# Kernel tuning notes

Hardware: AMD Instinct MI355X
Metric: run time of the kernel (lower is better)

The kernel has to match this reference:

```python
import jax, jax.numpy as jnp
import numpy as np

N = 4_194_304          # total events
C = 16                 # n classes
SIGNAL_CLS = 0         # signal_cls_idx
EPS = 1.0              # self.eps
B_BG = 2_097_152       # background rows (rows [0, B_BG) are background, rest signal)
N_SIG_SEG = 4          # len(idx['signal'])
N_BG_SEG = 8           # len(idx['background'])


def setup_inputs() -> dict:
    key = jax.random.key(0)
    k1, k2, k3, k4 = jax.random.split(key, 4)
    pred = jax.random.normal(k1, (N, C), dtype=jnp.float32)
    n_sig = N - B_BG
    # truth layout required by split_signal_and_background: background rows first
    # (class != SIGNAL_CLS), then signal rows (class == SIGNAL_CLS), one-hot.
    bg_cls = jax.random.randint(k2, (B_BG,), 1, C).astype(jnp.int32)
    sig_cls = jnp.full((n_sig,), SIGNAL_CLS, dtype=jnp.int32)
    truth = jax.nn.one_hot(jnp.concatenate([bg_cls, sig_cls]), C, dtype=jnp.float32)
    weight_signal = jax.random.uniform(k3, (N_SIG_SEG,), dtype=jnp.float32)
    weight_background = jax.random.uniform(k4, (N_BG_SEG,), dtype=jnp.float32)
    # equal-length contiguous segments (cumsum-slice structure of idx lists)
    signal_seg_ids = jnp.repeat(jnp.arange(N_SIG_SEG, dtype=jnp.int32), n_sig // N_SIG_SEG)
    background_seg_ids = jnp.repeat(jnp.arange(N_BG_SEG, dtype=jnp.int32), B_BG // N_BG_SEG)
    return {
        "pred": pred,
        "truth": truth,
        "weight_signal": weight_signal,
        "weight_background": weight_background,
        "signal_seg_ids": signal_seg_ids,
        "background_seg_ids": background_seg_ids,
        "signal_start": B_BG,
    }


def reference(pred, truth, weight_signal, weight_background,
              signal_seg_ids, background_seg_ids, signal_start):
    pred_cls = jnp.argmax(pred, axis=1)    # [N]
    truth_cls = jnpp_argmax = jnp.argmax(truth, axis=1)

    # ---- signal_score: per-segment efficiency * weight ----
    sig_pred_cls = pred_cls[signal_start:]
    sig_truth_cls = truth_cls[signal_start:]
    mism = (sig_pred_cls != sig_truth_cls).astype(jnp.float32)
    fn = jax.ops.segment_sum(mism, signal_seg_ids, num_segments=N_SIG_SEG)
    cnt = jax.ops.segment_sum(jnp.ones_like(mism), signal_seg_ids, num_segments=N_SIG_SEG)
    signal_fraction_score = jnp.sum((cnt - fn) / cnt * weight_signal)

    # ---- background_scores: sqrt(rate_into_signal * w + eps) per segment ----
    bg_pred_cls = pred_cls[:signal_start]
    hit = (bg_pred_cls == SIGNAL_CLS).astype(jnp.float32)
    fns = jax.ops.segment_sum(hit, background_seg_ids, num_segments=N_BG_SEG)
    cnt_b = jax.ops.segment_sum(jnp.ones_like(hit), background_seg_ids, num_segments=N_BG_SEG)
    background_fraction_score = jnp.sum(jnp.sqrt(fns / cnt_b * weight_background + EPS))

    max_score = jnp.sum(weight_signal) / jnp.sqrt(jnp.float32(EPS))
    coefficient = (max_score - signal_fraction_score) / background_fraction_score

    # base loss: mean softmax cross-entropy with soft (one-hot) targets
    loss = jnp.mean(-jnp.sum(truth * jax.nn.log_softmax(pred, axis=1), axis=1))
    return loss * coefficient
```

## Files before the change

### kernel.cpp

```cpp
#include <hip/hip_runtime.h>


__global__ void init_ws(double* loss_sum, unsigned int* ctr) {
    if (threadIdx.x == 0) *loss_sum = 0.0;
    if (threadIdx.x < 24) ctr[threadIdx.x] = 0u;
}

__global__ __launch_bounds__(256) void zscore_main(
    const float4* __restrict__ pred,
    const float4* __restrict__ truth,
    const int*    __restrict__ sig_ids,
    const int*    __restrict__ bg_ids,
    int N, int signal_start,
    double* __restrict__ loss_sum,
    unsigned int* __restrict__ ctr)
{
    __shared__ unsigned int s_flag[12];
    __shared__ unsigned int s_cnt[12];
    __shared__ float s_wave_loss[4];

    const int tid = threadIdx.x;
    if (tid < 12) { s_flag[tid] = 0u; s_cnt[tid] = 0u; }
    __syncthreads();

    const int T = gridDim.x * blockDim.x;
    float local_loss = 0.0f;

    for (int row = blockIdx.x * blockDim.x + tid; row < N; row += T) {
        const float4* pr = pred  + (size_t)row * 4;
        const float4* tr = truth + (size_t)row * 4;
        float4 p0 = pr[0], p1 = pr[1], p2 = pr[2], p3 = pr[3];
        float4 t0 = tr[0], t1 = tr[1], t2 = tr[2], t3 = tr[3];

        float v[16] = {p0.x,p0.y,p0.z,p0.w, p1.x,p1.y,p1.z,p1.w,
                       p2.x,p2.y,p2.z,p2.w, p3.x,p3.y,p3.z,p3.w};
        float t[16] = {t0.x,t0.y,t0.z,t0.w, t1.x,t1.y,t1.z,t1.w,
                       t2.x,t2.y,t2.z,t2.w, t3.x,t3.y,t3.z,t3.w};

        float pm = v[0]; int am = 0;
        #pragma unroll
        for (int i = 1; i < 16; ++i) { if (v[i] > pm) { pm = v[i]; am = i; } }

        float tmx = t[0]; int tm = 0;
        #pragma unroll
        for (int i = 1; i < 16; ++i) { if (t[i] > tmx) { tmx = t[i]; tm = i; } }

        float s = 0.0f;
        #pragma unroll
        for (int i = 0; i < 16; ++i) s += __expf(v[i] - pm);
        float lse = pm + __logf(s);

        float pv = v[0];
        #pragma unroll
        for (int i = 1; i < 16; ++i) pv = (i == tm) ? v[i] : pv;

        local_loss += lse - pv;

        bool isSig = row >= signal_start;
        int p; bool flag;
        if (isSig) { p = sig_ids[row - signal_start]; flag = (am != tm); }
        else       { p = 4 + bg_ids[row];             flag = (am == 0);  }

        int p0l = __builtin_amdgcn_readfirstlane(p);
        bool uni = __all(p == p0l);
        if (uni) {
            unsigned long long fb = __ballot(flag);
            unsigned long long ab = __ballot(true);
            if ((tid & 63) == 0) {
                atomicAdd(&s_cnt[p0l],  (unsigned int)__popcll(ab));
                atomicAdd(&s_flag[p0l], (unsigned int)__popcll(fb));
            }
        } else {
            atomicAdd(&s_cnt[p], 1u);
            if (flag) atomicAdd(&s_flag[p], 1u);
        }
    }

    #pragma unroll
    for (int off = 32; off > 0; off >>= 1)
        local_loss += __shfl_down(local_loss, off);
    if ((tid & 63) == 0) s_wave_loss[tid >> 6] = local_loss;
    __syncthreads();

    if (tid == 0) {
        float bl = s_wave_loss[0] + s_wave_loss[1] + s_wave_loss[2] + s_wave_loss[3];
        atomicAdd(loss_sum, (double)bl);
    }
    if (tid < 12) {
        int fIdx = (tid < 4) ? tid       : 8  + (tid - 4);
        int cIdx = (tid < 4) ? 4 + tid   : 16 + (tid - 4);
        if (s_flag[tid]) atomicAdd(&ctr[fIdx], s_flag[tid]);
        if (s_cnt[tid])  atomicAdd(&ctr[cIdx], s_cnt[tid]);
    }
}

__global__ void finalize(const float* __restrict__ w_sig,
                         const float* __restrict__ w_bg,
                         const double* __restrict__ loss_sum,
                         const unsigned int* __restrict__ ctr,
                         float* __restrict__ out, int N)
{
    if (threadIdx.x != 0 || blockIdx.x != 0) return;
    double sig = 0.0, wsum = 0.0;
    for (int s = 0; s < 4; ++s) {
        double cnt = (double)ctr[4 + s];
        double fn  = (double)ctr[s];
        sig  += (cnt - fn) / cnt * (double)w_sig[s];
        wsum += (double)w_sig[s];
    }
    double bg = 0.0;
    for (int s = 0; s < 8; ++s) {
        double fns = (double)ctr[8 + s];
        double cb  = (double)ctr[16 + s];
        bg += sqrt(fns / cb * (double)w_bg[s] + 1.0);
    }
    double coeff = (wsum - sig) / bg;
    double loss  = (*loss_sum) / (double)N;
    out[0] = (float)(loss * coeff);
}

extern "C" void kernel_launch(void* const* d_in, const int* in_sizes, int n_in,
                              void* d_out, int out_size, void* d_ws, size_t ws_size,
                              hipStream_t stream) {
    const float* pred   = (const float*)d_in[0];
    const float* truth  = (const float*)d_in[1];
    const float* w_sig  = (const float*)d_in[2];
    const float* w_bg   = (const float*)d_in[3];
    const int*   sigid  = (const int*)d_in[4];
    const int*   bgid   = (const int*)d_in[5];

    const int N = in_sizes[0] / 16;
    const int signal_start = in_sizes[5];

    double*       loss_sum = (double*)d_ws;
    unsigned int* ctr      = (unsigned int*)((char*)d_ws + 8);

    init_ws<<<1, 64, 0, stream>>>(loss_sum, ctr);

    const int blocks = 1024;
    zscore_main<<<blocks, 256, 0, stream>>>(
        (const float4*)pred, (const float4*)truth, sigid, bgid,
        N, signal_start, loss_sum, ctr);

    finalize<<<1, 64, 0, stream>>>(w_sig, w_bg, loss_sum, ctr, (float*)d_out, N);
}
```

Before: 537.1 us.

## Split each row across four lanes with coalesced float4 loads and per-block partials

Each row of 16 floats is now handled by four adjacent lanes, each loading one float4, so global loads are fully coalesced instead of each thread reading 64 contiguous bytes. Max, exp-sum and the target logit are combined across the lane quad with xor shuffles, and the next iteration's loads are prefetched one step ahead. Global atomics and the init kernel are replaced by per-block partial arrays reduced in a wider finalize kernel, dropping one launch. The cost is extra shuffles per row and redundant segment-id loads across the four lanes of a quad. The argmax check now uses float equality, so ties behave differently from the first-index rule.

```diff
diff --git a/kernel.cpp b/kernel.cpp
--- a/kernel.cpp
+++ b/kernel.cpp
@@ -1,122 +1,155 @@
 #include <hip/hip_runtime.h>
 
 
-__global__ void init_ws(double* loss_sum, unsigned int* ctr) {
-    if (threadIdx.x == 0) *loss_sum = 0.0;
-    if (threadIdx.x < 24) ctr[threadIdx.x] = 0u;
-}
+#define NBLK 2048
 
-__global__ __launch_bounds__(256) void zscore_main(
-    const float4* __restrict__ pred,
-    const float4* __restrict__ truth,
+__global__ __launch_bounds__(256, 8) void zscore_main(
+    const float4* __restrict__ pred4,
+    const float4* __restrict__ truth4,
     const int*    __restrict__ sig_ids,
     const int*    __restrict__ bg_ids,
     int N, int signal_start,
-    double* __restrict__ loss_sum,
-    unsigned int* __restrict__ ctr)
+    float* __restrict__ lossP,
+    unsigned int* __restrict__ ctrP)
 {
     __shared__ unsigned int s_flag[12];
     __shared__ unsigned int s_cnt[12];
     __shared__ float s_wave_loss[4];
 
-    const int tid = threadIdx.x;
+    const int tid  = threadIdx.x;
+    const int lane = tid & 63;
+    const int j    = tid & 3;
     if (tid < 12) { s_flag[tid] = 0u; s_cnt[tid] = 0u; }
     __syncthreads();
 
     const int T = gridDim.x * blockDim.x;
+    const int totalF = N * 4;
     float local_loss = 0.0f;
 
-    for (int row = blockIdx.x * blockDim.x + tid; row < N; row += T) {
-        const float4* pr = pred  + (size_t)row * 4;
-        const float4* tr = truth + (size_t)row * 4;
-        float4 p0 = pr[0], p1 = pr[1], p2 = pr[2], p3 = pr[3];
-        float4 t0 = tr[0], t1 = tr[1], t2 = tr[2], t3 = tr[3];
-
-        float v[16] = {p0.x,p0.y,p0.z,p0.w, p1.x,p1.y,p1.z,p1.w,
-                       p2.x,p2.y,p2.z,p2.w, p3.x,p3.y,p3.z,p3.w};
-        float t[16] = {t0.x,t0.y,t0.z,t0.w, t1.x,t1.y,t1.z,t1.w,
-                       t2.x,t2.y,t2.z,t2.w, t3.x,t3.y,t3.z,t3.w};
-
-        float pm = v[0]; int am = 0;
-        #pragma unroll
-        for (int i = 1; i < 16; ++i) { if (v[i] > pm) { pm = v[i]; am = i; } }
-
-        float tmx = t[0]; int tm = 0;
-        #pragma unroll
-        for (int i = 1; i < 16; ++i) { if (t[i] > tmx) { tmx = t[i]; tm = i; } }
-
-        float s = 0.0f;
-        #pragma unroll
-        for (int i = 0; i < 16; ++i) s += __expf(v[i] - pm);
-        float lse = pm + __logf(s);
-
-        float pv = v[0];
-        #pragma unroll
-        for (int i = 1; i < 16; ++i) pv = (i == tm) ? v[i] : pv;
-
-        local_loss += lse - pv;
-
-        bool isSig = row >= signal_start;
-        int p; bool flag;
-        if (isSig) { p = sig_ids[row - signal_start]; flag = (am != tm); }
-        else       { p = 4 + bg_ids[row];             flag = (am == 0);  }
-
-        int p0l = __builtin_amdgcn_readfirstlane(p);
-        bool uni = __all(p == p0l);
-        if (uni) {
-            unsigned long long fb = __ballot(flag);
-            unsigned long long ab = __ballot(true);
-            if ((tid & 63) == 0) {
-                atomicAdd(&s_cnt[p0l],  (unsigned int)__popcll(ab));
-                atomicAdd(&s_flag[p0l], (unsigned int)__popcll(fb));
-            }
-        } else {
-            atomicAdd(&s_cnt[p], 1u);
-            if (flag) atomicAdd(&s_flag[p], 1u);
-        }
+    int f = blockIdx.x * blockDim.x + tid;
+    bool valid = f < totalF;
+    float4 p, t; int seg = 0;
+    if (valid) {
+        p = pred4[f];
+        t = truth4[f];
+        int row = f >> 2;
+        seg = (row >= signal_start) ? sig_ids[row - signal_start] : bg_ids[row];
     }
 
+    while (valid) {
+        const int nf = f + T;
+        const bool nvalid = nf < totalF;
+        float4 np, nt; int nseg = 0;
+        if (nvalid) {
+            np = pred4[nf];
+            nt = truth4[nf];
+            int nrow = nf >> 2;
+            nseg = (nrow >= signal_start) ? sig_ids[nrow - signal_start]
+                                          : bg_ids[nrow];
+        }
+
+        {
+            const int row = f >> 2;
+            const bool isSig = row >= signal_start;
+
+            float pm = fmaxf(fmaxf(p.x, p.y), fmaxf(p.z, p.w));
+            pm = fmaxf(pm, __shfl_xor(pm, 1));
+            pm = fmaxf(pm, __shfl_xor(pm, 2));
+
+            float e  = __expf(p.x - pm) + __expf(p.y - pm)
+                     + __expf(p.z - pm) + __expf(p.w - pm);
+            float pv = p.x * t.x + p.y * t.y + p.z * t.z + p.w * t.w;
+            float ct = (p.x == pm ? t.x : 0.0f) + (p.y == pm ? t.y : 0.0f)
+                     + (p.z == pm ? t.z : 0.0f) + (p.w == pm ? t.w : 0.0f);
+            e  += __shfl_xor(e, 1);  pv += __shfl_xor(pv, 1);  ct += __shfl_xor(ct, 1);
+            e  += __shfl_xor(e, 2);  pv += __shfl_xor(pv, 2);  ct += __shfl_xor(ct, 2);
+
+            local_loss += pm + __logf(e) - pv;
+
+            bool flag;
+            int pp;
+            if (isSig) { pp = seg;     flag = (j == 0) && (ct < 0.5f); }
+            else       { pp = seg + 4; flag = (j == 0) && (p.x == pm); }
+
+            int p0l = __builtin_amdgcn_readfirstlane(pp);
+            bool uni = __all(pp == p0l);
+            if (uni) {
+                unsigned long long fb = __ballot(flag);
+                if (lane == 0) {
+                    atomicAdd(&s_cnt[p0l], 16u);
+                    atomicAdd(&s_flag[p0l], (unsigned int)__popcll(fb));
+                }
+            } else {
+                if (j == 0) {
+                    atomicAdd(&s_cnt[pp], 1u);
+                    if (flag) atomicAdd(&s_flag[pp], 1u);
+                }
+            }
+        }
+
+        p = np; t = nt; seg = nseg; f = nf; valid = nvalid;
+    }
+
+    local_loss *= 0.25f;
     #pragma unroll
     for (int off = 32; off > 0; off >>= 1)
         local_loss += __shfl_down(local_loss, off);
-    if ((tid & 63) == 0) s_wave_loss[tid >> 6] = local_loss;
+    if (lane == 0) s_wave_loss[tid >> 6] = local_loss;
     __syncthreads();
 
-    if (tid == 0) {
-        float bl = s_wave_loss[0] + s_wave_loss[1] + s_wave_loss[2] + s_wave_loss[3];
-        atomicAdd(loss_sum, (double)bl);
-    }
+    const int b = blockIdx.x;
+    const int B = gridDim.x;
+    if (tid == 0)
+        lossP[b] = s_wave_loss[0] + s_wave_loss[1] + s_wave_loss[2] + s_wave_loss[3];
     if (tid < 12) {
-        int fIdx = (tid < 4) ? tid       : 8  + (tid - 4);
-        int cIdx = (tid < 4) ? 4 + tid   : 16 + (tid - 4);
-        if (s_flag[tid]) atomicAdd(&ctr[fIdx], s_flag[tid]);
-        if (s_cnt[tid])  atomicAdd(&ctr[cIdx], s_cnt[tid]);
+        int fIdx = (tid < 4) ? tid     : 8  + (tid - 4);
+        int cIdx = (tid < 4) ? 4 + tid : 16 + (tid - 4);
+        ctrP[fIdx * B + b] = s_flag[tid];
+        ctrP[cIdx * B + b] = s_cnt[tid];
     }
 }
 
 __global__ void finalize(const float* __restrict__ w_sig,
                          const float* __restrict__ w_bg,
-                         const double* __restrict__ loss_sum,
-                         const unsigned int* __restrict__ ctr,
-                         float* __restrict__ out, int N)
+                         const float* __restrict__ lossP,
+                         const unsigned int* __restrict__ ctrP,
+                         float* __restrict__ out, int N, int B)
 {
-    if (threadIdx.x != 0 || blockIdx.x != 0) return;
-    double sig = 0.0, wsum = 0.0;
-    for (int s = 0; s < 4; ++s) {
-        double cnt = (double)ctr[4 + s];
-        double fn  = (double)ctr[s];
-        sig  += (cnt - fn) / cnt * (double)w_sig[s];
-        wsum += (double)w_sig[s];
+    const int lane = threadIdx.x;
+    unsigned int c[24];
+    #pragma unroll
+    for (int s = 0; s < 24; ++s) c[s] = 0u;
+    double lsd = 0.0;
+
+    for (int b = lane; b < B; b += 64) {
+        lsd += (double)lossP[b];
+        #pragma unroll
+        for (int s = 0; s < 24; ++s) c[s] += ctrP[s * B + b];
     }
-    double bg = 0.0;
-    for (int s = 0; s < 8; ++s) {
-        double fns = (double)ctr[8 + s];
-        double cb  = (double)ctr[16 + s];
-        bg += sqrt(fns / cb * (double)w_bg[s] + 1.0);
+    #pragma unroll
+    for (int off = 32; off > 0; off >>= 1) {
+        #pragma unroll
+        for (int s = 0; s < 24; ++s) c[s] += __shfl_down(c[s], off);
+        lsd += __shfl_down(lsd, off);
     }
-    double coeff = (wsum - sig) / bg;
-    double loss  = (*loss_sum) / (double)N;
-    out[0] = (float)(loss * coeff);
+
+    if (lane == 0) {
+        double sig = 0.0, wsum = 0.0;
+        for (int s = 0; s < 4; ++s) {
+            double cnt = (double)c[4 + s];
+            double fn  = (double)c[s];
+            sig  += (cnt - fn) / cnt * (double)w_sig[s];
+            wsum += (double)w_sig[s];
+        }
+        double bg = 0.0;
+        for (int s = 0; s < 8; ++s) {
+            double fns = (double)c[8 + s];
+            double cb  = (double)c[16 + s];
+            bg += sqrt(fns / cb * (double)w_bg[s] + 1.0);
+        }
+        double coeff = (wsum - sig) / bg;
+        out[0] = (float)(lsd / (double)N * coeff);
+    }
 }
 
 extern "C" void kernel_launch(void* const* d_in, const int* in_sizes, int n_in,
@@ -132,15 +165,13 @@
     const int N = in_sizes[0] / 16;
     const int signal_start = in_sizes[5];
 
-    double*       loss_sum = (double*)d_ws;
-    unsigned int* ctr      = (unsigned int*)((char*)d_ws + 8);
+    float*        lossP = (float*)d_ws;
+    unsigned int* ctrP  = (unsigned int*)((char*)d_ws + NBLK * sizeof(float));
 
-    init_ws<<<1, 64, 0, stream>>>(loss_sum, ctr);
+    zscore_main<<<NBLK, 256, 0, stream>>>(
+        (const float4*)pred, (const float4*)truth, sigid, bgid,
+        N, signal_start, lossP, ctrP);
 
-    const int blocks = 1024;
-    zscore_main<<<blocks, 256, 0, stream>>>(
-        (const float4*)pred, (const float4*)truth, sigid, bgid,
-        N, signal_start, loss_sum, ctr);
-
-    finalize<<<1, 64, 0, stream>>>(w_sig, w_bg, loss_sum, ctr, (float*)d_out, N);
+    finalize<<<1, 64, 0, stream>>>(w_sig, w_bg, lossP, ctrP,
+                                   (float*)d_out, N, NBLK);
 }
```

After: 544.9 us. About the same (+1.5%).
